# Kernel optimization log

Hardware: AMD Instinct MI355X
Metric: run time of the kernel (lower is better)

The kernel has to match this reference:

```python
import jax, jax.numpy as jnp
import numpy as np

OUT_F, IN_F = 4096, 4096
N_CLUSTERS = 256
B, S = 4, 2048


def setup_inputs() -> dict:
    key = jax.random.key(0)
    k1, k2, k3 = jax.random.split(key, 3)
    input_ = jax.random.normal(k1, (B, S, IN_F), dtype=jnp.float32)
    # centroid table: [n_clusters, 1] (embedding_dim = 1, scalar centroids)
    centroid_table = jax.random.normal(k2, (N_CLUSTERS, 1), dtype=jnp.float32) * 0.02
    # per-element centroid indices for the weight matrix [out_features, in_features]
    weight_idx = jax.random.randint(k3, (OUT_F, IN_F), 0, N_CLUSTERS, dtype=jnp.int32)
    return {"input_": input_, "centroid_table": centroid_table, "weight_idx": weight_idx}


def reference(input_, centroid_table, weight_idx):
    # Dequantize: gather scalar centroid per weight element -> [out_f, in_f]
    weights = centroid_table[:, 0][weight_idx]
    # F.linear(x, W): out = x @ W.T -> [B, S, out_f]
    out = jnp.einsum('bsi,oi->bso', input_, weights)
    return out
```

## Files before the change

kernel.cpp:

```cpp
#include <hip/hip_runtime.h>

typedef unsigned short u16;
typedef __attribute__((ext_vector_type(8))) __bf16 bf16x8;
typedef __attribute__((ext_vector_type(4))) float f32x4;
typedef __attribute__((ext_vector_type(4))) int i32x4;
typedef __attribute__((ext_vector_type(8))) unsigned short u16x8;

#define IN_F 4096
#define OUT_F 4096
#define MDIM 8192

__device__ __forceinline__ u16 f2bf(float f) {
  union { float f; unsigned int u; } v; v.f = f;
  unsigned int r = (v.u + 0x7fffu + ((v.u >> 16) & 1u)) >> 16;
  return (u16)r;
}

#define DQ_BLOCKS (OUT_F * IN_F / (8 * 256))
#define CV_BLOCKS (MDIM * IN_F / (8 * 256))

__global__ __launch_bounds__(256) void prep_kernel(const int* __restrict__ idx,
                                                   const float* __restrict__ table,
                                                   const float* __restrict__ X,
                                                   u16* __restrict__ Wb,
                                                   u16* __restrict__ Xb) {
  int b = blockIdx.x;
  if (b < DQ_BLOCKS) {
    __shared__ float cent[256];
    cent[threadIdx.x] = table[threadIdx.x];
    __syncthreads();
    size_t i = (size_t)b * 256 + threadIdx.x;
    const i32x4* p = (const i32x4*)idx + 2 * i;
    i32x4 v0 = __builtin_nontemporal_load(p);
    i32x4 v1 = __builtin_nontemporal_load(p + 1);
    u16x8 o;
    o[0] = f2bf(cent[v0[0]]); o[1] = f2bf(cent[v0[1]]);
    o[2] = f2bf(cent[v0[2]]); o[3] = f2bf(cent[v0[3]]);
    o[4] = f2bf(cent[v1[0]]); o[5] = f2bf(cent[v1[1]]);
    o[6] = f2bf(cent[v1[2]]); o[7] = f2bf(cent[v1[3]]);
    ((u16x8*)Wb)[i] = o;
  } else {
    size_t i = (size_t)(b - DQ_BLOCKS) * 256 + threadIdx.x;
    const f32x4* p = (const f32x4*)X + 2 * i;
    f32x4 v0 = __builtin_nontemporal_load(p);
    f32x4 v1 = __builtin_nontemporal_load(p + 1);
    u16x8 o;
    o[0] = f2bf(v0[0]); o[1] = f2bf(v0[1]); o[2] = f2bf(v0[2]); o[3] = f2bf(v0[3]);
    o[4] = f2bf(v1[0]); o[5] = f2bf(v1[1]); o[6] = f2bf(v1[2]); o[7] = f2bf(v1[3]);
    ((u16x8*)Xb)[i] = o;
  }
}

#define BM 256
#define BN 256
#define BK 64
#define NKT (IN_F / BK)

__device__ __forceinline__ void gld_lds16(const u16* g, u16* l) {
  __builtin_amdgcn_global_load_lds((const __attribute__((address_space(1))) void*)g,
                                   (__attribute__((address_space(3))) void*)l,
                                   16, 0, 0);
}

#define SBAR   __builtin_amdgcn_s_barrier()
#define LGKM0  asm volatile("s_waitcnt lgkmcnt(0)" ::: "memory")
#define VMCNT6 asm volatile("s_waitcnt vmcnt(6)" ::: "memory")
#define VMCNT0 asm volatile("s_waitcnt vmcnt(0)" ::: "memory")

#define STAGE2(SRC, DSTBASE)                                   \
  { const u16* _g = (SRC); u16* _l = (DSTBASE) + sdst;         \
    gld_lds16(_g, _l);                                         \
    gld_lds16(_g + (size_t)64 * IN_F, _l + 4096); }

#define LOAD_A(AF, HOFF)                                                   \
  _Pragma("unroll")                                                        \
  for (int mj = 0; mj < 4; ++mj) {                                         \
    AF[mj][0] = *(const bf16x8*)(Ac + (HOFF) + a_row + mj * 1024 + s0);    \
    AF[mj][1] = *(const bf16x8*)(Ac + (HOFF) + a_row + mj * 1024 + s1);    \
  }

#define LOAD_B(BF, HOFF)                                                   \
  _Pragma("unroll")                                                        \
  for (int nj = 0; nj < 2; ++nj) {                                         \
    BF[nj][0] = *(const bf16x8*)(Bc + (HOFF) + b_row + nj * 1024 + s0);    \
    BF[nj][1] = *(const bf16x8*)(Bc + (HOFF) + b_row + nj * 1024 + s1);    \
  }

#define MFMA_QUAD(AF, BF, MO, NO)                                          \
  _Pragma("unroll")                                                        \
  for (int mj = 0; mj < 4; ++mj) {                                         \
    _Pragma("unroll")                                                      \
    for (int nj = 0; nj < 2; ++nj) {                                       \
      acc[(MO) + mj][(NO) + nj] = __builtin_amdgcn_mfma_f32_16x16x32_bf16( \
          AF[mj][0], BF[nj][0], acc[(MO) + mj][(NO) + nj], 0, 0, 0);       \
      acc[(MO) + mj][(NO) + nj] = __builtin_amdgcn_mfma_f32_16x16x32_bf16( \
          AF[mj][1], BF[nj][1], acc[(MO) + mj][(NO) + nj], 0, 0, 0);       \
    }                                                                      \
  }

__global__ __launch_bounds__(512, 2) void gemm_kernel(const u16* __restrict__ Xb,
                                                      const u16* __restrict__ Wb,
                                                      float* __restrict__ out) {
  __shared__ __align__(16) u16 As[2][2 * 128 * BK];
  __shared__ __align__(16) u16 Bs[2][2 * 128 * BK];

  const int tid = threadIdx.x;
  const int lane = tid & 63;
  const int wv = tid >> 6;
  const int wm_i = wv >> 2;
  const int wn_i = wv & 3;

  const int orig = blockIdx.x;
  const int wgid = (orig & 7) * 64 + (orig >> 3);
  const int bm = wgid >> 4;
  const int bn = wgid & 15;

  const int schunk = ((tid & 7) - ((tid >> 4) & 7)) & 7;
  const size_t stg_off = (size_t)(tid >> 3) * IN_F + (size_t)schunk * 8;
  const u16* Ag = Xb + (size_t)bm * BM * IN_F + stg_off;
  const u16* Bg = Wb + (size_t)bn * BN * IN_F + stg_off;
  const int sdst = wv * 512;

  const int l15 = lane & 15;
  const int h4 = lane >> 4;
  const int hd = h4 + (l15 >> 1);
  const int s0 = (hd & 7) * 8;
  const int s1 = ((hd + 4) & 7) * 8;
  const int a_row = (wm_i * 64 + l15) * BK;
  const int b_row = (wn_i * 32 + l15) * BK;

  f32x4 acc[8][4] = {};
  bf16x8 a[4][2], b0[2][2], b1[2][2];

  STAGE2(Ag, As[0]);
  STAGE2(Bg, Bs[0]);
  STAGE2(Bg + (size_t)128 * IN_F, Bs[0] + 8192);
  STAGE2(Ag + (size_t)128 * IN_F, As[0] + 8192);
  STAGE2(Ag + BK, As[1]);
  STAGE2(Bg + BK, Bs[1]);
  STAGE2(Bg + (size_t)128 * IN_F + BK, Bs[1] + 8192);
  VMCNT6;
  SBAR;

  for (int kt = 0; kt < NKT; ++kt) {
    const u16* Ac = As[kt & 1];
    const u16* Bc = Bs[kt & 1];
    const size_t k1 = (size_t)((kt + 1 < NKT) ? kt + 1 : NKT - 1) * BK;
    const size_t k2 = (size_t)((kt + 2 < NKT) ? kt + 2 : NKT - 1) * BK;

    LOAD_A(a, 0);
    LOAD_B(b0, 0);
    STAGE2(Ag + (size_t)128 * IN_F + k1, As[(kt + 1) & 1] + 8192);
    SBAR; LGKM0;
    __builtin_amdgcn_s_setprio(1);
    MFMA_QUAD(a, b0, 0, 0);
    __builtin_amdgcn_s_setprio(0);
    SBAR;

    LOAD_B(b1, 8192);
    STAGE2(Ag + k2, As[kt & 1]);
    SBAR; LGKM0;
    __builtin_amdgcn_s_setprio(1);
    MFMA_QUAD(a, b1, 0, 2);
    __builtin_amdgcn_s_setprio(0);
    SBAR;

    LOAD_A(a, 8192);
    STAGE2(Bg + k2, Bs[kt & 1]);
    SBAR; LGKM0;
    __builtin_amdgcn_s_setprio(1);
    MFMA_QUAD(a, b1, 4, 2);
    __builtin_amdgcn_s_setprio(0);
    SBAR;

    STAGE2(Bg + (size_t)128 * IN_F + k2, Bs[kt & 1] + 8192);
    SBAR;
    __builtin_amdgcn_s_setprio(1);
    MFMA_QUAD(a, b0, 4, 0);
    __builtin_amdgcn_s_setprio(0);
    VMCNT6;
    SBAR;
  }

  VMCNT0;

  const size_t obase = (size_t)(bm * BM) * OUT_F + (size_t)(bn * BN) + (size_t)(wn_i * 32 + l15);
#pragma unroll
  for (int mi = 0; mi < 8; ++mi) {
    const int row = (mi >> 2) * 128 + wm_i * 64 + (mi & 3) * 16 + h4 * 4;
#pragma unroll
    for (int r = 0; r < 4; ++r) {
      float* op = out + obase + (size_t)(row + r) * OUT_F;
#pragma unroll
      for (int ni = 0; ni < 4; ++ni)
        __builtin_nontemporal_store(acc[mi][ni][r], op + (ni >> 1) * 128 + (ni & 1) * 16);
    }
  }
}

extern "C" void kernel_launch(void* const* d_in, const int* in_sizes, int n_in,
                              void* d_out, int out_size, void* d_ws, size_t ws_size,
                              hipStream_t stream) {
  const float* X = (const float*)d_in[0];
  const float* table = (const float*)d_in[1];
  const int* idx = (const int*)d_in[2];
  float* out = (float*)d_out;

  u16* Wb = (u16*)d_ws;
  u16* Xb = Wb + (size_t)OUT_F * IN_F;

  prep_kernel<<<DQ_BLOCKS + CV_BLOCKS, 256, 0, stream>>>(idx, table, X, Wb, Xb);
  gemm_kernel<<<(MDIM / BM) * (OUT_F / BN), 512, 0, stream>>>(Xb, Wb, out);
}
```

Before: 536.1 us.

## Split LDS tiles into K-halves and trim barriers in the GEMM main loop

```diff
diff --git a/kernel.cpp b/kernel.cpp
--- a/kernel.cpp
+++ b/kernel.cpp
@@ -63,27 +63,26 @@
 }
 
 #define SBAR   __builtin_amdgcn_s_barrier()
-#define LGKM0  asm volatile("s_waitcnt lgkmcnt(0)" ::: "memory")
 #define VMCNT6 asm volatile("s_waitcnt vmcnt(6)" ::: "memory")
 #define VMCNT0 asm volatile("s_waitcnt vmcnt(0)" ::: "memory")
 
 #define STAGE2(SRC, DSTBASE)                                   \
   { const u16* _g = (SRC); u16* _l = (DSTBASE) + sdst;         \
     gld_lds16(_g, _l);                                         \
-    gld_lds16(_g + (size_t)64 * IN_F, _l + 4096); }
+    gld_lds16(_g + 32, _l + 4096); }
 
 #define LOAD_A(AF, HOFF)                                                   \
   _Pragma("unroll")                                                        \
   for (int mj = 0; mj < 4; ++mj) {                                         \
-    AF[mj][0] = *(const bf16x8*)(Ac + (HOFF) + a_row + mj * 1024 + s0);    \
-    AF[mj][1] = *(const bf16x8*)(Ac + (HOFF) + a_row + mj * 1024 + s1);    \
+    AF[mj][0] = *(const bf16x8*)(Ac + (HOFF) + a_row + mj * 512 + s0);     \
+    AF[mj][1] = *(const bf16x8*)(Ac + (HOFF) + a_row + mj * 512 + 4096 + s0); \
   }
 
 #define LOAD_B(BF, HOFF)                                                   \
   _Pragma("unroll")                                                        \
   for (int nj = 0; nj < 2; ++nj) {                                         \
-    BF[nj][0] = *(const bf16x8*)(Bc + (HOFF) + b_row + nj * 1024 + s0);    \
-    BF[nj][1] = *(const bf16x8*)(Bc + (HOFF) + b_row + nj * 1024 + s1);    \
+    BF[nj][0] = *(const bf16x8*)(Bc + (HOFF) + b_row + nj * 512 + s0);     \
+    BF[nj][1] = *(const bf16x8*)(Bc + (HOFF) + b_row + nj * 512 + 4096 + s0); \
   }
 
 #define MFMA_QUAD(AF, BF, MO, NO)                                          \
@@ -115,71 +114,69 @@
   const int bm = wgid >> 4;
   const int bn = wgid & 15;
 
-  const int schunk = ((tid & 7) - ((tid >> 4) & 7)) & 7;
-  const size_t stg_off = (size_t)(tid >> 3) * IN_F + (size_t)schunk * 8;
+  const int srow = (tid >> 6) * 16 + (lane >> 2);
+  const int c0 = ((lane & 3) - ((lane >> 3) & 3)) & 3;
+  const size_t stg_off = (size_t)srow * IN_F + (size_t)c0 * 8;
   const u16* Ag = Xb + (size_t)bm * BM * IN_F + stg_off;
   const u16* Bg = Wb + (size_t)bn * BN * IN_F + stg_off;
   const int sdst = wv * 512;
 
   const int l15 = lane & 15;
   const int h4 = lane >> 4;
-  const int hd = h4 + (l15 >> 1);
-  const int s0 = (hd & 7) * 8;
-  const int s1 = ((hd + 4) & 7) * 8;
-  const int a_row = (wm_i * 64 + l15) * BK;
-  const int b_row = (wn_i * 32 + l15) * BK;
+  const int s0 = ((h4 + (l15 >> 1)) & 3) * 8;
+  const int a_row = (wm_i * 64 + l15) * 32;
+  const int b_row = (wn_i * 32 + l15) * 32;
 
   f32x4 acc[8][4] = {};
   bf16x8 a[4][2], b0[2][2], b1[2][2];
 
-  STAGE2(Ag, As[0]);
-  STAGE2(Bg, Bs[0]);
-  STAGE2(Bg + (size_t)128 * IN_F, Bs[0] + 8192);
-  STAGE2(Ag + (size_t)128 * IN_F, As[0] + 8192);
-  STAGE2(Ag + BK, As[1]);
-  STAGE2(Bg + BK, Bs[1]);
-  STAGE2(Bg + (size_t)128 * IN_F + BK, Bs[1] + 8192);
+  STAGE2(Ag, (u16*)As[0]);
+  STAGE2(Bg, (u16*)Bs[0]);
+  STAGE2(Bg + (size_t)128 * IN_F, (u16*)Bs[0] + 8192);
+  STAGE2(Ag + (size_t)128 * IN_F, (u16*)As[0] + 8192);
+  STAGE2(Ag + BK, (u16*)As[1]);
+  STAGE2(Bg + BK, (u16*)Bs[1]);
+  STAGE2(Bg + (size_t)128 * IN_F + BK, (u16*)Bs[1] + 8192);
   VMCNT6;
   SBAR;
 
   for (int kt = 0; kt < NKT; ++kt) {
     const u16* Ac = As[kt & 1];
     const u16* Bc = Bs[kt & 1];
+    u16* Ab = (u16*)As[kt & 1];
+    u16* An = (u16*)As[(kt + 1) & 1];
+    u16* Bb = (u16*)Bs[kt & 1];
     const size_t k1 = (size_t)((kt + 1 < NKT) ? kt + 1 : NKT - 1) * BK;
     const size_t k2 = (size_t)((kt + 2 < NKT) ? kt + 2 : NKT - 1) * BK;
 
     LOAD_A(a, 0);
     LOAD_B(b0, 0);
-    STAGE2(Ag + (size_t)128 * IN_F + k1, As[(kt + 1) & 1] + 8192);
-    SBAR; LGKM0;
+    STAGE2(Ag + (size_t)128 * IN_F + k1, An + 8192);
+    SBAR;
     __builtin_amdgcn_s_setprio(1);
     MFMA_QUAD(a, b0, 0, 0);
     __builtin_amdgcn_s_setprio(0);
-    SBAR;
 
     LOAD_B(b1, 8192);
-    STAGE2(Ag + k2, As[kt & 1]);
-    SBAR; LGKM0;
+    SBAR;
     __builtin_amdgcn_s_setprio(1);
     MFMA_QUAD(a, b1, 0, 2);
     __builtin_amdgcn_s_setprio(0);
-    SBAR;
 
     LOAD_A(a, 8192);
-    STAGE2(Bg + k2, Bs[kt & 1]);
-    SBAR; LGKM0;
+    STAGE2(Ag + k2, Ab);
+    SBAR;
     __builtin_amdgcn_s_setprio(1);
     MFMA_QUAD(a, b1, 4, 2);
     __builtin_amdgcn_s_setprio(0);
-    SBAR;
-
-    STAGE2(Bg + (size_t)128 * IN_F + k2, Bs[kt & 1] + 8192);
+
+    STAGE2(Bg + k2, Bb);
+    STAGE2(Bg + (size_t)128 * IN_F + k2, Bb + 8192);
+    VMCNT6;
     SBAR;
     __builtin_amdgcn_s_setprio(1);
     MFMA_QUAD(a, b0, 4, 0);
     __builtin_amdgcn_s_setprio(0);
-    VMCNT6;
-    SBAR;
   }
 
   VMCNT0;
```

Measured after the change: 476.4 us. -11.1%, faster.
